# Performance work log

Measured on AMD Instinct MI355X. Metric: run time of the kernel, lower is better.

## Reference

```python
import jax, jax.numpy as jnp
import numpy as np
from jax import lax

DIM = 256
NI, NS, NP = 8, 4, 16
H = W = 36
SCALE = 20.0
POOL = 4
EPS_BN = 1e-5


def setup_inputs() -> dict:
    key = jax.random.key(0)
    ks = jax.random.split(key, 20)
    feat = jax.random.normal(ks[0], (NI, NS, DIM, H, W), jnp.float32)
    # proposals in xywh; scaled by 20 inside PrRoIPool, so keep boxes inside the 36x36 map
    xy = jax.random.uniform(ks[1], (NI, NS, NP, 2), jnp.float32) * 1.2
    wh = 0.1 + jax.random.uniform(ks[2], (NI, NS, NP, 2), jnp.float32) * 0.4
    proposals = jnp.concatenate([xy, wh], axis=-1)

    def kaiming(k, shape, fan_in):
        return jax.random.normal(k, shape, jnp.float32) * np.float32(np.sqrt(2.0 / fan_in))

    d = dict(feat=feat, proposals=proposals)
    for i, name in enumerate(['conv1', 'conv2', 'conv3']):
        d[name + '_w'] = kaiming(ks[3 + i], (DIM, DIM, 3, 3), DIM * 9)
        d[name + '_b'] = jnp.zeros((DIM,), jnp.float32)
        d['bn%d_g' % (i + 1)] = jax.random.uniform(ks[6 + i], (DIM,), jnp.float32)
        d['bn%d_b' % (i + 1)] = jnp.zeros((DIM,), jnp.float32)
    d['fc_w'] = kaiming(ks[9], (DIM, DIM * POOL * POOL), DIM * POOL * POOL)
    d['fc_b'] = jnp.zeros((DIM,), jnp.float32)
    d['fcbn_g'] = jax.random.uniform(ks[10], (DIM,), jnp.float32)
    d['fcbn_b'] = jnp.zeros((DIM,), jnp.float32)
    d['iou_w'] = kaiming(ks[11], (1, DIM), DIM)
    d['iou_b'] = jnp.zeros((1,), jnp.float32)
    return d


def _cbr(x, w, b, g, beta):
    # Conv(3x3, pad 1) + BatchNorm (training-mode batch stats) + ReLU
    x = lax.conv_general_dilated(x, w, (1, 1), ((1, 1), (1, 1)),
                                 dimension_numbers=('NCHW', 'OIHW', 'NCHW'))
    x = x + b[None, :, None, None]
    m = x.mean((0, 2, 3), keepdims=True)
    v = x.var((0, 2, 3), keepdims=True)
    x = (x - m) / jnp.sqrt(v + EPS_BN) * g[None, :, None, None] + beta[None, :, None, None]
    return jax.nn.relu(x)


def _trapcum_last(a):
    # trapezoidal cumulative integral along last axis, value 0 at index 0
    mid = 0.5 * (a[..., :-1] + a[..., 1:])
    return jnp.concatenate([jnp.zeros_like(a[..., :1]), jnp.cumsum(mid, axis=-1)], axis=-1)


def _prroi_pool(feat, rois, pooled=POOL, scale=SCALE):
    # Precise RoI pooling: exact double integral of the bilinear interpolant per bin,
    # computed analytically via trapezoidal cumulative integrals of the feature map.
    N, C, Hh, Ww = feat.shape
    Ux = _trapcum_last(feat)                                            # int_0^x f
    Uy = jnp.swapaxes(_trapcum_last(jnp.swapaxes(feat, -1, -2)), -1, -2)  # int_0^y f
    T = jnp.swapaxes(_trapcum_last(jnp.swapaxes(Ux, -1, -2)), -1, -2)     # int_0^y int_0^x f

    b = rois[:, 0].astype(jnp.int32)
    x1, y1, x2, y2 = (rois[:, 1] * scale, rois[:, 2] * scale,
                      rois[:, 3] * scale, rois[:, 4] * scale)
    bw = (x2 - x1) / pooled
    bh = (y2 - y1) / pooled
    grid = jnp.arange(pooled + 1, dtype=feat.dtype)
    xs = jnp.clip(x1[:, None] + bw[:, None] * grid, 0.0, Ww - 1)        # (R, P+1)
    ys = jnp.clip(y1[:, None] + bh[:, None] * grid, 0.0, Hh - 1)
    wx = jnp.clip(jnp.floor(xs), 0, Ww - 2).astype(jnp.int32)
    hy = jnp.clip(jnp.floor(ys), 0, Hh - 2).astype(jnp.int32)
    sx = xs - wx.astype(feat.dtype)
    sy = ys - hy.astype(feat.dtype)
    px1 = 0.5 * sx * sx
    px0 = sx - px1
    py1 = 0.5 * sy * sy
    py0 = sy - py1

    def g(arr, hi, wi):
        # gather per-RoI values -> (R, P+1, P+1, C), rows index y, cols index x
        return arr[b[:, None, None], :, hi[:, :, None], wi[:, None, :]]

    px0e = px0[:, None, :, None]
    px1e = px1[:, None, :, None]
    py0e = py0[:, :, None, None]
    py1e = py1[:, :, None, None]
    h0, h1 = hy, hy + 1
    w0, w1 = wx, wx + 1
    # antiderivative G(X, Y) = int_0^Y int_0^X f of the bilinear interpolant
    G = (g(T, h0, w0)
         + g(Uy, h0, w0) * px0e + g(Uy, h0, w1) * px1e
         + py0e * (g(Ux, h0, w0) + g(feat, h0, w0) * px0e + g(feat, h0, w1) * px1e)
         + py1e * (g(Ux, h1, w0) + g(feat, h1, w0) * px0e + g(feat, h1, w1) * px1e))
    # per-bin integral via inclusion-exclusion on the (P+1)x(P+1) corner grid
    d = G[:, 1:, 1:] - G[:, :-1, 1:] - G[:, 1:, :-1] + G[:, :-1, :-1]   # (R, P, P, C)
    area = (bw * bh)[:, None, None, None]
    out = jnp.where(area > 1e-8, d / jnp.maximum(area, 1e-8), 0.0)
    return jnp.transpose(out, (0, 3, 1, 2))  # (R, C, P, P)


def reference(feat, proposals, conv1_w, conv1_b, bn1_g, bn1_b, conv2_w, conv2_b,
              bn2_g, bn2_b, conv3_w, conv3_b, bn3_g, bn3_b, fc_w, fc_b,
              fcbn_g, fcbn_b, iou_w, iou_b):
    ni, ns = proposals.shape[0], proposals.shape[1]
    x = feat.reshape(-1, *feat.shape[-3:])
    x = _cbr(x, conv1_w, conv1_b, bn1_g, bn1_b)
    x = _cbr(x, conv2_w, conv2_b, bn2_g, bn2_b)
    x = _cbr(x, conv3_w, conv3_b, bn3_g, bn3_b)

    props = proposals.reshape(ni * ns, -1, 4)
    B, P = props.shape[0], props.shape[1]
    xyxy = jnp.concatenate([props[..., 0:2], props[..., 0:2] + props[..., 2:4]], axis=-1)
    bidx = jnp.broadcast_to(jnp.arange(B, dtype=props.dtype)[:, None, None], (B, P, 1))
    rois = jnp.concatenate([bidx, xyxy], axis=-1).reshape(-1, 5)

    rf = _prroi_pool(x, rois)                       # (B*P, C, 4, 4)
    fcx = rf.reshape(rf.shape[0], -1) @ fc_w.T + fc_b
    m = fcx.mean(0)
    v = fcx.var(0)
    fcx = jax.nn.relu((fcx - m) / jnp.sqrt(v + EPS_BN) * fcbn_g + fcbn_b)
    iou = fcx @ iou_w.T + iou_b                     # (B*P, 1)
    return iou.reshape(ni, ns, -1)
```

## Files before the change

### kernel.cpp

```cpp
#include <hip/hip_runtime.h>
#include <hip/hip_bf16.h>
#include <stdint.h>

#define CDIM 256
#define HH 36
#define WW 36
#define NPX 1296
#define PW 38
#define PPIX 1444
#define NIMG 32
#define NROI 512
#define FCK 4096
#define EPS_BN 1e-5f
#define SBLK 192

typedef __bf16 bf16;
typedef __bf16 bf16x8 __attribute__((ext_vector_type(8)));
typedef float f32x4 __attribute__((ext_vector_type(4)));
typedef unsigned short us8 __attribute__((ext_vector_type(8)));

#define GLD16(g, l) __builtin_amdgcn_global_load_lds( \
    (__attribute__((address_space(1))) void*)(g),     \
    (__attribute__((address_space(3))) void*)(l), 16, 0, 0)

__global__ void k_wconv3(const float* __restrict__ w0, const float* __restrict__ w1,
                         const float* __restrict__ w2, bf16* __restrict__ wb) {
  int l = blockIdx.y;
  const float* ws = (l == 0) ? w0 : (l == 1) ? w1 : w2;
  bf16* dst = wb + (size_t)l * 9 * CDIM * CDIM;
  int i = blockIdx.x * 256 + threadIdx.x;
  if (i >= 9 * CDIM * CDIM) return;
  int tap = i / (CDIM * CDIM);
  int rem = i - tap * (CDIM * CDIM);
  int co = rem >> 8, ci = rem & 255;
  dst[i] = (bf16)ws[(size_t)(co * CDIM + ci) * 9 + tap];
}

__global__ void k_cast(const float* __restrict__ src, bf16* __restrict__ dst, int nElem) {
  int i = blockIdx.x * 256 + threadIdx.x;
  if (i < nElem) dst[i] = (bf16)src[i];
}

__global__ void k_convert(const float* __restrict__ feat, bf16* __restrict__ xp) {
  __shared__ bf16 tile[CDIM * 38];
  int h = blockIdx.x, n = blockIdx.y, t = threadIdx.x;
  const float* src = feat + (size_t)n * CDIM * NPX + (size_t)h * WW;
#pragma unroll 4
  for (int i = 0; i < 36; ++i) {
    int f = i * 256 + t;
    int c = (int)(((unsigned)f * 7282u) >> 18);
    int w = f - c * 36;
    tile[c * 38 + w] = (bf16)src[(size_t)c * NPX + w];
  }
  __syncthreads();
  bf16* dst = xp + (size_t)n * PPIX * CDIM + ((h + 1) * PW + 1) * CDIM + t;
#pragma unroll 4
  for (int w = 0; w < 36; ++w) dst[w * CDIM] = tile[t * 38 + w];
}

__global__ __launch_bounds__(256) void k_conv(
    const bf16* __restrict__ xp, const bf16* __restrict__ wb,
    bf16* __restrict__ y)
{
  __shared__ __align__(16) bf16 ldsA[2][4096];
  __shared__ __align__(16) bf16 ldsB[2][4096];
  const int tid = threadIdx.x;
  const int wave = tid >> 6, lane = tid & 63;
  const int pxt = blockIdx.x, cot = blockIdx.y, n = blockIdx.z;

  const int q = lane >> 2;
  const int gsw = (lane & 3) ^ ((q >> 1) & 3);
  const int rA = wave * 32 + q;
  const bf16* aS0 = wb + (size_t)(cot * 128 + rA) * CDIM + gsw * 8;
  const bf16* aS1 = aS0 + 16 * CDIM;
  int pxa = pxt * 128 + rA;       if (pxa > NPX - 1) pxa = NPX - 1;
  int pxb = pxt * 128 + rA + 16;  if (pxb > NPX - 1) pxb = NPX - 1;
  const int ha = pxa / 36, wa = pxa - ha * 36;
  const int hb = pxb / 36, wbv = pxb - hb * 36;
  const bf16* bS0 = xp + (size_t)n * (PPIX * CDIM) + ((ha + 1) * PW + (wa + 1)) * CDIM + gsw * 8;
  const bf16* bS1 = xp + (size_t)n * (PPIX * CDIM) + ((hb + 1) * PW + (wbv + 1)) * CDIM + gsw * 8;

  const int fr = lane & 15, fg = lane >> 4;
  const int fsw = (fg ^ ((fr >> 1) & 3)) * 8;
  const int wco = wave >> 1, wpx = wave & 1;
  const int aoff = (wco * 64 + fr) * 32 + fsw;
  const int boff = (wpx * 64 + fr) * 32 + fsw;

  f32x4 acc[4][4];
#pragma unroll
  for (int i = 0; i < 4; ++i)
#pragma unroll
    for (int j = 0; j < 4; ++j) acc[i][j] = f32x4{0.f, 0.f, 0.f, 0.f};

  {
    const int xoff = -(PW + 1) * CDIM;
    GLD16(aS0, &ldsA[0][wave * 1024]);
    GLD16(aS1, &ldsA[0][wave * 1024 + 512]);
    GLD16(bS0 + xoff, &ldsB[0][wave * 1024]);
    GLD16(bS1 + xoff, &ldsB[0][wave * 1024 + 512]);
  }

#pragma unroll 2
  for (int k = 0; k < 72; ++k) {
    const int buf = k & 1;
    __syncthreads();
    if (k + 1 < 72) {
      const int kn = k + 1;
      const int tap = kn >> 3, ci0 = (kn & 7) << 5;
      const int dh = tap / 3 - 1, dw = tap - (tap / 3) * 3 - 1;
      const int woff = tap * (CDIM * CDIM) + ci0;
      const int xoff = (dh * PW + dw) * CDIM + ci0;
      const int nb = buf ^ 1;
      GLD16(aS0 + woff, &ldsA[nb][wave * 1024]);
      GLD16(aS1 + woff, &ldsA[nb][wave * 1024 + 512]);
      GLD16(bS0 + xoff, &ldsB[nb][wave * 1024]);
      GLD16(bS1 + xoff, &ldsB[nb][wave * 1024 + 512]);
    }
    bf16x8 av[4], bv[4];
#pragma unroll
    for (int i = 0; i < 4; ++i) av[i] = *(const bf16x8*)&ldsA[buf][aoff + i * 512];
#pragma unroll
    for (int j = 0; j < 4; ++j) bv[j] = *(const bf16x8*)&ldsB[buf][boff + j * 512];
#pragma unroll
    for (int i = 0; i < 4; ++i)
#pragma unroll
      for (int j = 0; j < 4; ++j)
        acc[i][j] = __builtin_amdgcn_mfma_f32_16x16x32_bf16(av[i], bv[j], acc[i][j], 0, 0, 0);
  }

#pragma unroll
  for (int j = 0; j < 4; ++j) {
    const int px = pxt * 128 + wpx * 64 + j * 16 + fr;
    if (px < NPX) {
      bf16* dst = y + ((size_t)n * NPX + px) * CDIM + cot * 128 + wco * 64 + fg * 4;
#pragma unroll
      for (int i = 0; i < 4; ++i) {
        f32x4 a = acc[i][j];
        union { bf16 b4[4]; ushort4 u4; } pk;
        pk.b4[0] = (bf16)a[0]; pk.b4[1] = (bf16)a[1];
        pk.b4[2] = (bf16)a[2]; pk.b4[3] = (bf16)a[3];
        *(ushort4*)(dst + i * 16) = pk.u4;
      }
    }
  }
}

__global__ void k_statsb(const bf16* __restrict__ y, float* __restrict__ psum,
                         float* __restrict__ psq) {
  __shared__ float lsum[8][256];
  __shared__ float lsq[8][256];
  int t = threadIdx.x;
  int c8 = (t & 31) * 8, rg = t >> 5;
  size_t row0 = (size_t)blockIdx.x * 216 + rg;
  float s[8], qq[8];
#pragma unroll
  for (int k = 0; k < 8; ++k) { s[k] = 0.f; qq[k] = 0.f; }
  for (int i = 0; i < 27; ++i) {
    const bf16* p = y + (row0 + (size_t)i * 8) * CDIM + c8;
    union { bf16 b8[8]; us8 u; } v;
    v.u = *(const us8*)p;
#pragma unroll
    for (int k = 0; k < 8; ++k) {
      float f = (float)v.b8[k];
      s[k] += f; qq[k] += f * f;
    }
  }
#pragma unroll
  for (int k = 0; k < 8; ++k) { lsum[rg][c8 + k] = s[k]; lsq[rg][c8 + k] = qq[k]; }
  __syncthreads();
  float ss = 0.f, sq2 = 0.f;
#pragma unroll
  for (int g = 0; g < 8; ++g) { ss += lsum[g][t]; sq2 += lsq[g][t]; }
  psum[blockIdx.x * 256 + t] = ss;
  psq[blockIdx.x * 256 + t] = sq2;
}

__global__ void k_sred(const float* __restrict__ psum, const float* __restrict__ psq,
                       float* __restrict__ su, float* __restrict__ sq) {
  int c = threadIdx.x;
  float s = 0.f, q = 0.f;
  for (int i = 0; i < SBLK; ++i) { s += psum[i * 256 + c]; q += psq[i * 256 + c]; }
  su[c] = s; sq[c] = q;
}

__global__ void k_stats(const float* __restrict__ x, float* __restrict__ sum,
                        float* __restrict__ ssq, int rpb) {
  int c = threadIdx.x;
  size_t base = (size_t)blockIdx.x * rpb;
  float s = 0.f, s2 = 0.f;
  for (int i = 0; i < rpb; ++i) {
    float v = x[(base + i) * CDIM + c];
    s += v; s2 += v * v;
  }
  atomicAdd(&sum[c], s);
  atomicAdd(&ssq[c], s2);
}

__global__ void k_finalize(const float* __restrict__ sum, const float* __restrict__ ssq,
                           const float* __restrict__ g, const float* __restrict__ b,
                           float* __restrict__ sc, float* __restrict__ sh, float invn) {
  int c = threadIdx.x;
  float m = sum[c] * invn;
  float v = ssq[c] * invn - m * m;
  float s = g[c] * rsqrtf(v + EPS_BN);
  sc[c] = s;
  sh[c] = b[c] - m * s;
}

__global__ void k_normalize(const bf16* __restrict__ y, const float* __restrict__ sc,
                            const float* __restrict__ sh, bf16* __restrict__ xp) {
  int t = threadIdx.x;
  int n = blockIdx.y;
  int px = blockIdx.x * 8 + (t >> 5);
  int c8 = (t & 31) * 8;
  const bf16* srcp = y + ((size_t)n * NPX + px) * CDIM + c8;
  union { bf16 b8[8]; us8 u; } in, outp;
  in.u = *(const us8*)srcp;
  int h = px / 36, w = px - h * 36;
#pragma unroll
  for (int i = 0; i < 8; ++i) {
    float v = (float)in.b8[i];
    outp.b8[i] = (bf16)fmaxf(v * sc[c8 + i] + sh[c8 + i], 0.f);
  }
  *(us8*)(xp + (size_t)n * PPIX * CDIM + ((h + 1) * PW + (w + 1)) * CDIM + c8) = outp.u;
}

__device__ __forceinline__ float hatH(float u) {
  u = fminf(fmaxf(u, -1.f), 1.f);
  float p = u + 1.f;
  return (u < 0.f) ? 0.5f * p * p : 0.5f + u * (1.f - 0.5f * u);
}

__global__ __launch_bounds__(128) void k_pool(
    const bf16* __restrict__ y, const float* __restrict__ sc,
    const float* __restrict__ sh, const float* __restrict__ props,
    bf16* __restrict__ rf) {
  int roi = blockIdx.x;
  int c = blockIdx.y * 128 + threadIdx.x;
  int b = roi >> 4;
  const float* pr = props + (size_t)roi * 4;
  float x1 = pr[0] * 20.f, yy1 = pr[1] * 20.f;
  float x2 = (pr[0] + pr[2]) * 20.f, yy2 = (pr[1] + pr[3]) * 20.f;
  float bw = (x2 - x1) * 0.25f, bh = (yy2 - yy1) * 0.25f;

  float xs[5], ys[5];
#pragma unroll
  for (int j = 0; j < 5; ++j) {
    xs[j] = fminf(fmaxf(x1 + bw * j, 0.f), 35.f);
    ys[j] = fminf(fmaxf(yy1 + bh * j, 0.f), 35.f);
  }
  float wxv[4][5], wyv[4][5];
  int sx[4], sy[4];
#pragma unroll
  for (int j = 0; j < 4; ++j) {
    float a = xs[j], bb = xs[j + 1];
    int s = (int)floorf(a);
    sx[j] = s;
#pragma unroll
    for (int k = 0; k < 5; ++k) {
      float w = (float)(s + k);
      wxv[j][k] = hatH(bb - w) - hatH(a - w);
    }
    float ay = ys[j], by = ys[j + 1];
    int t = (int)floorf(ay);
    sy[j] = t;
#pragma unroll
    for (int k = 0; k < 5; ++k) {
      float w = (float)(t + k);
      wyv[j][k] = hatH(by - w) - hatH(ay - w);
    }
  }

  float s_ = sc[c], t_ = sh[c];
  const bf16* yb = y + (size_t)b * NPX * CDIM + c;
  float acc[4][4];
#pragma unroll
  for (int i = 0; i < 4; ++i)
#pragma unroll
    for (int j = 0; j < 4; ++j) acc[i][j] = 0.f;

#pragma unroll
  for (int i = 0; i < 4; ++i) {
#pragma unroll
    for (int ky = 0; ky < 5; ++ky) {
      float wy = wyv[i][ky];
      if (wy == 0.f) continue;
      int h = sy[i] + ky; if (h > 35) h = 35;
      const bf16* rowp = yb + h * (WW * CDIM);
#pragma unroll
      for (int j = 0; j < 4; ++j) {
        float rd = 0.f;
#pragma unroll
        for (int kx = 0; kx < 5; ++kx) {
          int w = sx[j] + kx; if (w > 35) w = 35;
          float f = fmaxf((float)rowp[w * CDIM] * s_ + t_, 0.f);
          rd += wxv[j][kx] * f;
        }
        acc[i][j] += wy * rd;
      }
    }
  }

  float area = bw * bh;
  float inv = area > 1e-8f ? 1.f / area : 0.f;
  bf16 outv[16];
#pragma unroll
  for (int i = 0; i < 4; ++i)
#pragma unroll
    for (int j = 0; j < 4; ++j)
      outv[i * 4 + j] = (bf16)(acc[i][j] * inv);
  bf16* dst = rf + (size_t)roi * FCK + c * 16;
  *(us8*)(dst)     = *(us8*)&outv[0];
  *(us8*)(dst + 8) = *(us8*)&outv[8];
}

__global__ __launch_bounds__(256) void k_fcgemm(const bf16* __restrict__ rf,
                                                const bf16* __restrict__ fw,
                                                float* __restrict__ fcp) {
  int tid = threadIdx.x, wave = tid >> 6, lane = tid & 63;
  int wo = wave >> 1, wr = wave & 1;
  int rt = blockIdx.x, ot = blockIdx.y, ks = blockIdx.z;
  int fr = lane & 15, fg = lane >> 4;
  const bf16* ap = fw + (size_t)(ot * 64 + wo * 32 + fr) * FCK + ks * 512 + fg * 8;
  const bf16* bp = rf + (size_t)(rt * 64 + wr * 32 + fr) * FCK + ks * 512 + fg * 8;
  f32x4 acc[2][2];
#pragma unroll
  for (int i = 0; i < 2; ++i)
#pragma unroll
    for (int j = 0; j < 2; ++j) acc[i][j] = f32x4{0.f, 0.f, 0.f, 0.f};
#pragma unroll 4
  for (int k = 0; k < 512; k += 32) {
    bf16x8 a0 = *(const bf16x8*)(ap + k);
    bf16x8 a1 = *(const bf16x8*)(ap + 16 * FCK + k);
    bf16x8 b0 = *(const bf16x8*)(bp + k);
    bf16x8 b1 = *(const bf16x8*)(bp + 16 * FCK + k);
    acc[0][0] = __builtin_amdgcn_mfma_f32_16x16x32_bf16(a0, b0, acc[0][0], 0, 0, 0);
    acc[0][1] = __builtin_amdgcn_mfma_f32_16x16x32_bf16(a0, b1, acc[0][1], 0, 0, 0);
    acc[1][0] = __builtin_amdgcn_mfma_f32_16x16x32_bf16(a1, b0, acc[1][0], 0, 0, 0);
    acc[1][1] = __builtin_amdgcn_mfma_f32_16x16x32_bf16(a1, b1, acc[1][1], 0, 0, 0);
  }
#pragma unroll
  for (int i = 0; i < 2; ++i)
#pragma unroll
    for (int j = 0; j < 2; ++j) {
      int o = ot * 64 + wo * 32 + i * 16 + fg * 4;
      int r = rt * 64 + wr * 32 + j * 16 + fr;
      *(f32x4*)(fcp + ((size_t)ks * NROI + r) * CDIM + o) = acc[i][j];
    }
}

__global__ void k_fcred(const float* __restrict__ fcp, float* __restrict__ fcx) {
  int r = blockIdx.x, o = threadIdx.x;
  float s = 0.f;
#pragma unroll
  for (int ks = 0; ks < 8; ++ks) s += fcp[((size_t)ks * NROI + r) * CDIM + o];
  fcx[(size_t)r * CDIM + o] = s;
}

__global__ void k_iou(const float* __restrict__ fcx, const float* __restrict__ sc,
                      const float* __restrict__ sh, const float* __restrict__ iw,
                      const float* __restrict__ ib, float* __restrict__ out) {
  __shared__ float red[4];
  int roi = blockIdx.x, t = threadIdx.x;
  float v = fcx[(size_t)roi * CDIM + t];
  v = fmaxf(v * sc[t] + sh[t], 0.f) * iw[t];
#pragma unroll
  for (int o = 32; o > 0; o >>= 1) v += __shfl_down(v, o);
  if ((t & 63) == 0) red[t >> 6] = v;
  __syncthreads();
  if (t == 0) out[roi] = red[0] + red[1] + red[2] + red[3] + ib[0];
}

extern "C" void kernel_launch(void* const* d_in, const int* in_sizes, int n_in,
                              void* d_out, int out_size, void* d_ws, size_t ws_size,
                              hipStream_t stream) {
  (void)in_sizes; (void)n_in; (void)out_size;
  const float* feat  = (const float*)d_in[0];
  const float* props = (const float*)d_in[1];
  const float* convw[3] = {(const float*)d_in[2], (const float*)d_in[6], (const float*)d_in[10]};
  const float* bng[3]   = {(const float*)d_in[4], (const float*)d_in[8], (const float*)d_in[12]};
  const float* bnb[3]   = {(const float*)d_in[5], (const float*)d_in[9], (const float*)d_in[13]};
  const float* fcw  = (const float*)d_in[14];
  const float* fcg  = (const float*)d_in[16];
  const float* fcbb = (const float*)d_in[17];
  const float* iw   = (const float*)d_in[18];
  const float* ib   = (const float*)d_in[19];
  float* out = (float*)d_out;

  char* w = (char*)d_ws;
  size_t off = 0;
  auto take = [&](size_t sz) -> char* { char* p = w + off; off += (sz + 255) & ~(size_t)255; return p; };
  const size_t SZ_XP = (size_t)NIMG * PPIX * CDIM * 2;
  const size_t SZ_YB = (size_t)NIMG * NPX * CDIM * 2;
  const size_t SZ_P  = (size_t)SBLK * 256 * 4;
  bf16*  xp0 = (bf16*)take(SZ_XP);
  bf16*  xp1 = (bf16*)take(SZ_XP);
  bf16*  y   = (bf16*)take(SZ_YB);
  bf16*  wball = (bf16*)take((size_t)3 * 9 * CDIM * CDIM * 2);
  bf16*  fwb = (bf16*)take((size_t)CDIM * FCK * 2);
  bf16*  rfb = (bf16*)take((size_t)NROI * FCK * 2);
  float* fcx = (float*)take((size_t)NROI * CDIM * 4);
  float* fcp = (float*)take((size_t)8 * NROI * CDIM * 4);
  float* psum = (float*)take(SZ_P);
  float* psq  = (float*)take(SZ_P);
  float* stat = (float*)take(8 * 256 * 4);
  float* scsh = (float*)take(8 * 256 * 4);
  if (off > ws_size) return;

  hipMemsetAsync(xp0, 0, SZ_XP * 2, stream);
  hipMemsetAsync(stat, 0, 8 * 256 * 4, stream);

  k_wconv3<<<dim3(2304, 3), 256, 0, stream>>>(convw[0], convw[1], convw[2], wball);
  k_cast<<<dim3(4096), 256, 0, stream>>>(fcw, fwb, CDIM * FCK);
  k_convert<<<dim3(HH, NIMG), 256, 0, stream>>>(feat, xp0);

  for (int l = 0; l < 3; ++l) {
    bf16* xin = (l == 1) ? xp1 : xp0;
    bf16* wbl = wball + (size_t)l * 9 * CDIM * CDIM;
    k_conv<<<dim3(11, 2, NIMG), 256, 0, stream>>>(xin, wbl, y);
    float* su = stat + l * 512; float* sq = su + 256;
    k_statsb<<<dim3(SBLK), 256, 0, stream>>>(y, psum, psq);
    k_sred<<<dim3(1), 256, 0, stream>>>(psum, psq, su, sq);
    float* sc = scsh + l * 512; float* sh = sc + 256;
    k_finalize<<<dim3(1), 256, 0, stream>>>(su, sq, bng[l], bnb[l], sc, sh, 1.f / 41472.f);
    if (l < 2) {
      bf16* xo = (l == 0) ? xp1 : xp0;
      k_normalize<<<dim3(NPX / 8, NIMG), 256, 0, stream>>>(y, sc, sh, xo);
    }
  }
  float* sc3 = scsh + 2 * 512; float* sh3 = sc3 + 256;
  k_pool<<<dim3(NROI, 2), 128, 0, stream>>>(y, sc3, sh3, props, rfb);
  k_fcgemm<<<dim3(8, 4, 8), 256, 0, stream>>>(rfb, fwb, fcp);
  k_fcred<<<dim3(NROI), 256, 0, stream>>>(fcp, fcx);
  float* fsu = stat + 3 * 512; float* fsq = fsu + 256;
  k_stats<<<dim3(8), 256, 0, stream>>>(fcx, fsu, fsq, 64);
  float* fsc = scsh + 3 * 512; float* fsh = fsc + 256;
  k_finalize<<<dim3(1), 256, 0, stream>>>(fsu, fsq, fcg, fcbb, fsc, fsh, 1.f / 512.f);
  k_iou<<<dim3(NROI), 256, 0, stream>>>(fcx, fsc, fsh, iw, ib, out);
}
```

Measured before the change: 490.2 us.

## Flatten conv pixel tiling across images, swizzle blocks, fuse stat reduce with finalize

```diff
diff --git a/kernel.cpp b/kernel.cpp
--- a/kernel.cpp
+++ b/kernel.cpp
@@ -13,6 +13,7 @@
 #define FCK 4096
 #define EPS_BN 1e-5f
 #define SBLK 192
+#define GPXT 324
 
 typedef __bf16 bf16;
 typedef __bf16 bf16x8 __attribute__((ext_vector_type(8)));
@@ -66,19 +67,26 @@
   __shared__ __align__(16) bf16 ldsB[2][4096];
   const int tid = threadIdx.x;
   const int wave = tid >> 6, lane = tid & 63;
-  const int pxt = blockIdx.x, cot = blockIdx.y, n = blockIdx.z;
+
+  const int B = blockIdx.x;
+  const int g = (B & 7) * 81 + (B >> 3);
+  const int cot = g / GPXT, gpxt = g - cot * GPXT;
 
   const int q = lane >> 2;
   const int gsw = (lane & 3) ^ ((q >> 1) & 3);
   const int rA = wave * 32 + q;
   const bf16* aS0 = wb + (size_t)(cot * 128 + rA) * CDIM + gsw * 8;
   const bf16* aS1 = aS0 + 16 * CDIM;
-  int pxa = pxt * 128 + rA;       if (pxa > NPX - 1) pxa = NPX - 1;
-  int pxb = pxt * 128 + rA + 16;  if (pxb > NPX - 1) pxb = NPX - 1;
-  const int ha = pxa / 36, wa = pxa - ha * 36;
-  const int hb = pxb / 36, wbv = pxb - hb * 36;
-  const bf16* bS0 = xp + (size_t)n * (PPIX * CDIM) + ((ha + 1) * PW + (wa + 1)) * CDIM + gsw * 8;
-  const bf16* bS1 = xp + (size_t)n * (PPIX * CDIM) + ((hb + 1) * PW + (wbv + 1)) * CDIM + gsw * 8;
+  const int gpx0 = gpxt * 128 + rA;
+  const int gpx1 = gpx0 + 16;
+  const int n0 = (int)(((unsigned)gpx0 * 51782u) >> 26);
+  const int n1 = (int)(((unsigned)gpx1 * 51782u) >> 26);
+  const int p0 = gpx0 - n0 * 1296, p1 = gpx1 - n1 * 1296;
+  const int h0 = (int)(((unsigned)p0 * 7282u) >> 18);
+  const int h1 = (int)(((unsigned)p1 * 7282u) >> 18);
+  const int w0 = p0 - h0 * 36, w1 = p1 - h1 * 36;
+  const bf16* bS0 = xp + (size_t)n0 * (PPIX * CDIM) + ((h0 + 1) * PW + (w0 + 1)) * CDIM + gsw * 8;
+  const bf16* bS1 = xp + (size_t)n1 * (PPIX * CDIM) + ((h1 + 1) * PW + (w1 + 1)) * CDIM + gsw * 8;
 
   const int fr = lane & 15, fg = lane >> 4;
   const int fsw = (fg ^ ((fr >> 1) & 3)) * 8;
@@ -130,17 +138,15 @@
 
 #pragma unroll
   for (int j = 0; j < 4; ++j) {
-    const int px = pxt * 128 + wpx * 64 + j * 16 + fr;
-    if (px < NPX) {
-      bf16* dst = y + ((size_t)n * NPX + px) * CDIM + cot * 128 + wco * 64 + fg * 4;
-#pragma unroll
-      for (int i = 0; i < 4; ++i) {
-        f32x4 a = acc[i][j];
-        union { bf16 b4[4]; ushort4 u4; } pk;
-        pk.b4[0] = (bf16)a[0]; pk.b4[1] = (bf16)a[1];
-        pk.b4[2] = (bf16)a[2]; pk.b4[3] = (bf16)a[3];
-        *(ushort4*)(dst + i * 16) = pk.u4;
-      }
+    const int gpx = gpxt * 128 + wpx * 64 + j * 16 + fr;
+    bf16* dst = y + (size_t)gpx * CDIM + cot * 128 + wco * 64 + fg * 4;
+#pragma unroll
+    for (int i = 0; i < 4; ++i) {
+      f32x4 a = acc[i][j];
+      union { bf16 b4[4]; ushort4 u4; } pk;
+      pk.b4[0] = (bf16)a[0]; pk.b4[1] = (bf16)a[1];
+      pk.b4[2] = (bf16)a[2]; pk.b4[3] = (bf16)a[3];
+      *(ushort4*)(dst + i * 16) = pk.u4;
     }
   }
 }
@@ -175,12 +181,17 @@
   psq[blockIdx.x * 256 + t] = sq2;
 }
 
-__global__ void k_sred(const float* __restrict__ psum, const float* __restrict__ psq,
-                       float* __restrict__ su, float* __restrict__ sq) {
+__global__ void k_sredfin(const float* __restrict__ psum, const float* __restrict__ psq,
+                          const float* __restrict__ g, const float* __restrict__ b,
+                          float* __restrict__ sc, float* __restrict__ sh, float invn) {
   int c = threadIdx.x;
   float s = 0.f, q = 0.f;
   for (int i = 0; i < SBLK; ++i) { s += psum[i * 256 + c]; q += psq[i * 256 + c]; }
-  su[c] = s; sq[c] = q;
+  float m = s * invn;
+  float v = q * invn - m * m;
+  float sca = g[c] * rsqrtf(v + EPS_BN);
+  sc[c] = sca;
+  sh[c] = b[c] - m * sca;
 }
 
 __global__ void k_stats(const float* __restrict__ x, float* __restrict__ sum,
@@ -417,12 +428,10 @@
   for (int l = 0; l < 3; ++l) {
     bf16* xin = (l == 1) ? xp1 : xp0;
     bf16* wbl = wball + (size_t)l * 9 * CDIM * CDIM;
-    k_conv<<<dim3(11, 2, NIMG), 256, 0, stream>>>(xin, wbl, y);
-    float* su = stat + l * 512; float* sq = su + 256;
+    k_conv<<<dim3(648), 256, 0, stream>>>(xin, wbl, y);
     k_statsb<<<dim3(SBLK), 256, 0, stream>>>(y, psum, psq);
-    k_sred<<<dim3(1), 256, 0, stream>>>(psum, psq, su, sq);
     float* sc = scsh + l * 512; float* sh = sc + 256;
-    k_finalize<<<dim3(1), 256, 0, stream>>>(su, sq, bng[l], bnb[l], sc, sh, 1.f / 41472.f);
+    k_sredfin<<<dim3(1), 256, 0, stream>>>(psum, psq, bng[l], bnb[l], sc, sh, 1.f / 41472.f);
     if (l < 2) {
       bf16* xo = (l == 0) ? xp1 : xp0;
       k_normalize<<<dim3(NPX / 8, NIMG), 256, 0, stream>>>(y, sc, sh, xo);
```

Measured after the change: 488.0 us. About the same (-0.5%).
